# Kernel optimization log

Hardware: AMD Instinct MI355X
Metric: run time of the kernel (lower is better)

Reference implementation:

```python
import jax, jax.numpy as jnp
import numpy as np

N_NODES = 50000
N_EDGES = 800000
NFEAT, NHID, NCLASS, NCLUSTER = 512, 64, 16, 32


def gcn_conv(x, W, b, edge_index, edge_weight, n):
    """PyG GCNConv: add self-loops, symmetric normalization, linear + scatter-add."""
    row, col = edge_index[0], edge_index[1]
    loop = jnp.arange(n, dtype=row.dtype)
    row = jnp.concatenate([row, loop])
    col = jnp.concatenate([col, loop])
    w = jnp.concatenate([edge_weight, jnp.ones((n,), dtype=edge_weight.dtype)])
    # degree computed on target index (gcn_norm convention)
    deg = jax.ops.segment_sum(w, col, num_segments=n)
    dinv = jnp.where(deg > 0, jax.lax.rsqrt(deg), 0.0)
    norm = dinv[row] * w * dinv[col]          # [E+n]
    xw = x @ W                                # [n, out]
    msg = xw[row] * norm[:, None]             # gather + scale
    out = jax.ops.segment_sum(msg, col, num_segments=n)  # scatter-add
    return out + b


def setup_inputs() -> dict:
    key = jax.random.key(0)
    ks = jax.random.split(key, 12)
    def glorot(k, fan_in, fan_out):
        s = np.sqrt(6.0 / (fan_in + fan_out)).astype(np.float32)
        return jax.random.uniform(k, (fan_in, fan_out), jnp.float32, -s, s)
    x = jax.random.normal(ks[0], (N_NODES, NFEAT), jnp.float32)
    edge_index = jax.random.randint(ks[1], (2, N_EDGES), 0, N_NODES, dtype=jnp.int64)
    edge_weight = jax.random.uniform(ks[2], (N_EDGES,), jnp.float32)
    return {
        "x": x, "edge_index": edge_index, "edge_weight": edge_weight,
        "W1": glorot(ks[3], NFEAT, NHID), "b1": jnp.zeros((NHID,), jnp.float32),
        "W2": glorot(ks[4], NHID, NHID), "b2": jnp.zeros((NHID,), jnp.float32),
        "fcW1": glorot(ks[5], NHID, NCLASS), "fcb1": jnp.zeros((NCLASS,), jnp.float32),
        "fcW2": glorot(ks[6], NHID, NCLUSTER), "fcb2": jnp.zeros((NCLUSTER,), jnp.float32),
    }


def reference(x, edge_index, edge_weight, W1, b1, W2, b2, fcW1, fcb1, fcW2, fcb2):
    n = x.shape[0]
    h = jax.nn.relu(gcn_conv(x, W1, b1, edge_index, edge_weight, n))
    # dropout omitted (eval-mode / deterministic reference)
    h = gcn_conv(h, W2, b2, edge_index, edge_weight, n)
    pred = h @ fcW1 + fcb1
    pred_cluster = h @ fcW2 + fcb2
    return (pred, pred_cluster)
```

## Files before the change

### kernel.cpp

```cpp
#include <hip/hip_runtime.h>
#include <hip/hip_bf16.h>
#include <cstdint>
#include <cstddef>

#define N_FEAT 512
#define N_HID 64
#define N_CLASS 16
#define N_CLUSTER 32
#define NPART 8

typedef short short8 __attribute__((ext_vector_type(8)));
typedef float floatx4 __attribute__((ext_vector_type(4)));
typedef unsigned short u16;
typedef unsigned short u16x4 __attribute__((ext_vector_type(4)));

__device__ __forceinline__ short f2bf(float f) {
  __hip_bfloat16 h = __float2bfloat16(f);
  return *reinterpret_cast<short*>(&h);
}
__device__ __forceinline__ u16 f2bfu(float f) { return (u16)f2bf(f); }
__device__ __forceinline__ float bf2f(u16 u) {
  return __uint_as_float((unsigned)u << 16);
}

__global__ void k_zeroH(uint4* __restrict__ p, int n16) {
  int i = blockIdx.x * 256 + threadIdx.x;
  if (i < n16) p[i] = make_uint4(0u, 0u, 0u, 0u);
}

__global__ void k_degcnt2(const int* __restrict__ col, const float* __restrict__ w,
                          unsigned long long* __restrict__ hist, int H, int E) {
  int e = blockIdx.x * 256 + threadIdx.x;
  if (e >= E) return;
  int p = blockIdx.x & (NPART - 1);
  int c = col[e];
  unsigned long long fx = (unsigned long long)__float2uint_rn(w[e] * 16777216.0f);
  atomicAdd(&hist[(size_t)p * H + c], (1ull << 40) | fx);
}

__global__ void k_reduce(const unsigned long long* __restrict__ hist, int H,
                         int* __restrict__ cnt, float* __restrict__ dinv, int n) {
  int i = blockIdx.x * 256 + threadIdx.x;
  if (i >= n) return;
  unsigned long long tot = 0;
  #pragma unroll
  for (int p = 0; p < NPART; ++p) tot += hist[(size_t)p * H + i];
  int c = (int)(tot >> 40);
  float wsum = (float)(tot & ((1ull << 40) - 1)) * 5.9604644775390625e-08f;
  cnt[i] = c;
  dinv[i] = rsqrtf(1.0f + wsum);
}

__global__ __launch_bounds__(256) void k_scan1(const int* __restrict__ cnt,
                                               int* __restrict__ off,
                                               int* __restrict__ bsum, int n) {
  __shared__ int sh[256];
  int t = threadIdx.x;
  int i = blockIdx.x * 256 + t;
  int v = (i < n) ? cnt[i] : 0;
  sh[t] = v;
  __syncthreads();
  #pragma unroll
  for (int d = 1; d < 256; d <<= 1) {
    int x = 0;
    if (t >= d) x = sh[t - d];
    __syncthreads();
    if (t >= d) sh[t] += x;
    __syncthreads();
  }
  if (i < n) off[i] = sh[t] - v;
  if (t == 255) bsum[blockIdx.x] = sh[255];
}

__global__ __launch_bounds__(256) void k_scan2(const int* __restrict__ bsum,
                                               int* __restrict__ bsum2, int nb) {
  __shared__ int sh[256];
  int t = threadIdx.x;
  int v = (t < nb) ? bsum[t] : 0;
  sh[t] = v;
  __syncthreads();
  #pragma unroll
  for (int d = 1; d < 256; d <<= 1) {
    int x = 0;
    if (t >= d) x = sh[t - d];
    __syncthreads();
    if (t >= d) sh[t] += x;
    __syncthreads();
  }
  if (t < nb) bsum2[t] = sh[t] - v;
}

__global__ void k_scan3_initcur(int* __restrict__ off, const int* __restrict__ bsum2,
                                const unsigned long long* __restrict__ hist, int H,
                                int* __restrict__ cur, int n, int E) {
  int i = blockIdx.x * 256 + threadIdx.x;
  if (i < n) {
    int o = off[i] + bsum2[blockIdx.x];
    off[i] = o;
    int running = o;
    #pragma unroll
    for (int p = 0; p < NPART; ++p) {
      cur[(size_t)p * H + i] = running;
      running += (int)(hist[(size_t)p * H + i] >> 40);
    }
  }
  if (i == 0) off[n] = E;
}

__global__ void k_fill2(const int* __restrict__ rowi, const int* __restrict__ coli,
                        const float* __restrict__ w, const float* __restrict__ dinv,
                        int* __restrict__ cur, int H,
                        unsigned* __restrict__ pairs, int E) {
  int e = blockIdx.x * 256 + threadIdx.x;
  if (e >= E) return;
  int p = blockIdx.x & (NPART - 1);
  int r = rowi[e], c = coli[e];
  int pos = atomicAdd(&cur[(size_t)p * H + c], 1);
  unsigned pk = ((unsigned)r << 16) | (u16)f2bf(dinv[r] * w[e] * dinv[c]);
  pairs[pos] = pk;
}

__global__ void k_prepBF(const float* __restrict__ W, short* __restrict__ BF, int K) {
  int idx = blockIdx.x * 256 + threadIdx.x;
  int total = (K / 32) * 4 * 64;
  if (idx >= total) return;
  int lane = idx & 63;
  int sj = idx >> 6;
  int j = sj & 3, s = sj >> 2;
  int col = j * 16 + (lane & 15);
  int k0 = s * 32 + ((lane >> 4) << 3);
  short8 v;
  #pragma unroll
  for (int t = 0; t < 8; ++t) v[t] = f2bf(W[(size_t)(k0 + t) * 64 + col]);
  *(short8*)(BF + (size_t)idx * 8) = v;
}

template<int K, bool ABF>
__global__ __launch_bounds__(64, 4) void k_mfma(
    const void* __restrict__ Av, const short8* __restrict__ BF,
    u16* __restrict__ C, int M) {
  constexpr int NSTEP = K / 32;
  constexpr int PA = (NSTEP < 4) ? NSTEP : 4;
  constexpr int PB = (NSTEP < 2) ? NSTEP : 2;
  const int lane = threadIdx.x & 63;
  const int rbase = blockIdx.x * 16;
  int r = rbase + (lane & 15);
  if (r >= M) r = M - 1;
  const int klo = (lane >> 4) * 8;
  const float* arowf = (const float*)Av + (size_t)r * K + klo;
  const u16*   arowh = (const u16*)Av + (size_t)r * K + klo;
  const short8* bbase = BF + lane;

  float4 pa0[PA], pa1[PA];
  short8 pah[PA];
  short8 pb[PB][4];
  #pragma unroll
  for (int s = 0; s < PA; ++s) {
    if constexpr (ABF) {
      pah[s] = *(const short8*)(arowh + s * 32);
    } else {
      pa0[s] = *(const float4*)(arowf + s * 32);
      pa1[s] = *(const float4*)(arowf + s * 32 + 4);
    }
  }
  #pragma unroll
  for (int s = 0; s < PB; ++s) {
    #pragma unroll
    for (int j = 0; j < 4; ++j)
      pb[s][j] = bbase[(s * 4 + j) * 64];
  }
  __builtin_amdgcn_sched_barrier(0);

  floatx4 acc[4];
  #pragma unroll
  for (int j = 0; j < 4; ++j) acc[j] = (floatx4){0.f, 0.f, 0.f, 0.f};

  #pragma unroll
  for (int s = 0; s < NSTEP; ++s) {
    const int sa = s % PA;
    const int sb = s % PB;
    short8 af;
    if constexpr (ABF) {
      af = pah[sa];
    } else {
      float4 a0 = pa0[sa], a1 = pa1[sa];
      af[0] = f2bf(a0.x); af[1] = f2bf(a0.y); af[2] = f2bf(a0.z); af[3] = f2bf(a0.w);
      af[4] = f2bf(a1.x); af[5] = f2bf(a1.y); af[6] = f2bf(a1.z); af[7] = f2bf(a1.w);
    }
    acc[0] = __builtin_amdgcn_mfma_f32_16x16x32_bf16(af, pb[sb][0], acc[0], 0, 0, 0);
    acc[1] = __builtin_amdgcn_mfma_f32_16x16x32_bf16(af, pb[sb][1], acc[1], 0, 0, 0);
    acc[2] = __builtin_amdgcn_mfma_f32_16x16x32_bf16(af, pb[sb][2], acc[2], 0, 0, 0);
    acc[3] = __builtin_amdgcn_mfma_f32_16x16x32_bf16(af, pb[sb][3], acc[3], 0, 0, 0);
    if (s + PA < NSTEP) {
      if constexpr (ABF) {
        pah[sa] = *(const short8*)(arowh + (s + PA) * 32);
      } else {
        pa0[sa] = *(const float4*)(arowf + (s + PA) * 32);
        pa1[sa] = *(const float4*)(arowf + (s + PA) * 32 + 4);
      }
    }
    if (s + PB < NSTEP) {
      #pragma unroll
      for (int j = 0; j < 4; ++j)
        pb[sb][j] = bbase[((s + PB) * 4 + j) * 64];
    }
    __builtin_amdgcn_sched_barrier(0);
  }

  const int srow = rbase + (lane >> 4) * 4;
  const int scol = lane & 15;
  #pragma unroll
  for (int i = 0; i < 4; ++i) {
    int rr = srow + i;
    if (rr < M) {
      #pragma unroll
      for (int j = 0; j < 4; ++j)
        C[(size_t)rr * 64 + j * 16 + scol] = f2bfu(acc[j][i]);
    }
  }
}

template<bool RELU>
__global__ __launch_bounds__(256) void k_gather(
    const int* __restrict__ off, const unsigned* __restrict__ pairs,
    const float* __restrict__ dinv,
    const u16* __restrict__ xw, const float* __restrict__ bias,
    u16* __restrict__ h, int n) {
  int gid = blockIdx.x * 256 + threadIdx.x;
  int c = gid >> 6, lane = gid & 63;
  if (c >= n) return;
  float s = dinv[c]; s *= s;
  float acc = fmaf(bf2f(xw[(size_t)c * 64 + lane]), s, bias[lane]);
  int i = off[c], end = off[c + 1];
  for (; i + 7 < end; i += 8) {
    unsigned p[8];
    float v[8];
    #pragma unroll
    for (int t = 0; t < 8; ++t) p[t] = pairs[i + t];
    #pragma unroll
    for (int t = 0; t < 8; ++t)
      v[t] = bf2f(xw[(size_t)(p[t] >> 16) * 64 + lane]);
    #pragma unroll
    for (int t = 0; t < 8; ++t)
      acc = fmaf(v[t], __uint_as_float((p[t] & 0xffffu) << 16), acc);
  }
  for (; i + 1 < end; i += 2) {
    unsigned p0 = pairs[i], p1 = pairs[i + 1];
    float v0 = bf2f(xw[(size_t)(p0 >> 16) * 64 + lane]);
    float v1 = bf2f(xw[(size_t)(p1 >> 16) * 64 + lane]);
    acc = fmaf(v0, __uint_as_float((p0 & 0xffffu) << 16), acc);
    acc = fmaf(v1, __uint_as_float((p1 & 0xffffu) << 16), acc);
  }
  if (i < end) {
    unsigned p = pairs[i];
    acc = fmaf(bf2f(xw[(size_t)(p >> 16) * 64 + lane]),
               __uint_as_float((p & 0xffffu) << 16), acc);
  }
  if (RELU) acc = fmaxf(acc, 0.f);
  h[(size_t)c * 64 + lane] = f2bfu(acc);
}

__global__ __launch_bounds__(256) void k_fc(
    const u16* __restrict__ h,
    const float* __restrict__ fW1, const float* __restrict__ fb1,
    const float* __restrict__ fW2, const float* __restrict__ fb2,
    float* __restrict__ out, int M) {
  __shared__ float Hs[64][68];
  __shared__ float Ws[64][48];
  __shared__ float bs[48];
  const int t = threadIdx.x;
  const int row0 = blockIdx.x * 64;
  #pragma unroll
  for (int i = 0; i < 4; ++i) {
    int f = t + i * 256;
    int r = f >> 4, k4 = f & 15;
    int rr = row0 + r;
    float4 v = make_float4(0.f, 0.f, 0.f, 0.f);
    if (rr < M) {
      u16x4 u = *(const u16x4*)&h[(size_t)rr * 64 + k4 * 4];
      v = make_float4(bf2f(u[0]), bf2f(u[1]), bf2f(u[2]), bf2f(u[3]));
    }
    *(float4*)&Hs[r][k4 * 4] = v;
  }
  for (int f = t; f < 64 * 48; f += 256) {
    int k = f / 48, c = f - k * 48;
    Ws[k][c] = (c < 16) ? fW1[k * 16 + c] : fW2[k * 32 + (c - 16)];
  }
  if (t < 48) bs[t] = (t < 16) ? fb1[t] : fb2[t - 16];
  __syncthreads();
  const int tr = t >> 4, tc = t & 15;
  float acc[4][3] = {{0.f}};
  #pragma unroll 8
  for (int k = 0; k < 64; ++k) {
    float a[4], b[3];
    #pragma unroll
    for (int i = 0; i < 4; ++i) a[i] = Hs[tr * 4 + i][k];
    #pragma unroll
    for (int j = 0; j < 3; ++j) b[j] = Ws[k][tc * 3 + j];
    #pragma unroll
    for (int i = 0; i < 4; ++i)
      #pragma unroll
      for (int j = 0; j < 3; ++j) acc[i][j] = fmaf(a[i], b[j], acc[i][j]);
  }
  #pragma unroll
  for (int i = 0; i < 4; ++i) {
    int rr = row0 + tr * 4 + i;
    if (rr >= M) continue;
    #pragma unroll
    for (int j = 0; j < 3; ++j) {
      int c = tc * 3 + j;
      float v = acc[i][j] + bs[c];
      if (c < 16) out[(size_t)rr * 16 + c] = v;
      else out[(size_t)M * 16 + (size_t)rr * 32 + (c - 16)] = v;
    }
  }
}

extern "C" void kernel_launch(void* const* d_in, const int* in_sizes, int n_in,
                              void* d_out, int out_size, void* d_ws, size_t ws_size,
                              hipStream_t stream) {
  const float* x    = (const float*)d_in[0];
  const int*   ei   = (const int*)d_in[1];
  const float* ew   = (const float*)d_in[2];
  const float* W1   = (const float*)d_in[3];
  const float* b1   = (const float*)d_in[4];
  const float* W2   = (const float*)d_in[5];
  const float* b2   = (const float*)d_in[6];
  const float* fW1  = (const float*)d_in[7];
  const float* fb1  = (const float*)d_in[8];
  const float* fW2  = (const float*)d_in[9];
  const float* fb2  = (const float*)d_in[10];
  float* out = (float*)d_out;

  const int N = in_sizes[0] / N_FEAT;
  const int E = in_sizes[2];
  const int H = (N + 63) & ~63;
  const int* row = ei;
  const int* col = ei + E;

  char* ws = (char*)d_ws;
  float*              dinv = (float*)(ws + 0x000000);
  int*                cnt  = (int*)  (ws + 0x040000);
  int*                off  = (int*)  (ws + 0x080000);
  int*                bsum = (int*)  (ws + 0x0C0000);
  int*                bsum2= (int*)  (ws + 0x0C1000);
  short*              BF1  = (short*)(ws + 0x0C8000);
  short*              BF2  = (short*)(ws + 0x0DA000);
  unsigned long long* hist = (unsigned long long*)(ws + 0x100000);
  int*                cur  = (int*)  (ws + 0x500000);
  unsigned*           pairs= (unsigned*)(ws + 0x6C0000);
  u16*                bufA = (u16*)  (ws + 0xD40000);
  u16*                bufB = (u16*)  (ws + 0x1980000);

  const int nbN  = (N + 255) / 256;
  const int nbE  = (E + 255) / 256;
  const int nbT  = (N + 15) / 16;
  const int nbG  = (N + 63) / 64;
  const int nbW  = (N * 64 + 255) / 256;
  const int nH16 = NPART * H / 2;
  const int nbZ  = (nH16 + 255) / 256;

  k_prepBF<<<32, 256, 0, stream>>>(W1, BF1, N_FEAT);
  k_prepBF<<<2,  256, 0, stream>>>(W2, BF2, N_HID);

  k_zeroH  <<<nbZ, 256, 0, stream>>>((uint4*)hist, nH16);
  k_degcnt2<<<nbE, 256, 0, stream>>>(col, ew, hist, H, E);
  k_reduce <<<nbN, 256, 0, stream>>>(hist, H, cnt, dinv, N);
  k_scan1  <<<nbN, 256, 0, stream>>>(cnt, off, bsum, N);
  k_scan2  <<<1,   256, 0, stream>>>(bsum, bsum2, nbN);
  k_scan3_initcur<<<nbN, 256, 0, stream>>>(off, bsum2, hist, H, cur, N, E);
  k_fill2  <<<nbE, 256, 0, stream>>>(row, col, ew, dinv, cur, H, pairs, E);

  k_mfma<N_FEAT, false><<<nbT, 64, 0, stream>>>(x, (const short8*)BF1, bufA, N);
  k_gather<true><<<nbW, 256, 0, stream>>>(off, pairs, dinv, bufA, b1, bufB, N);

  k_mfma<N_HID, true><<<nbT, 64, 0, stream>>>(bufB, (const short8*)BF2, bufA, N);
  k_gather<false><<<nbW, 256, 0, stream>>>(off, pairs, dinv, bufA, b2, bufB, N);

  k_fc<<<nbG, 256, 0, stream>>>(bufB, fW1, fb1, fW2, fb2, out, N);
}
```

Baseline: 196.6 us.

## Stage x tiles through swizzled LDS with double buffering in first GEMM

Replaces the single-wave 16-row MFMA kernel for the 512-wide input projection with a 256-thread, 64-row block. Each block streams 64-column fp32 chunks of x into XOR-swizzled double-buffered shared memory with coalesced loads, then each wave converts to bf16 and issues MFMAs while the next chunk loads. The K=64 second GEMM is split into its own simplified kernel. The aim is better global-load coalescing and more memory parallelism on the 100MB x read, at the cost of barriers and LDS traffic.

```diff
diff --git a/kernel.cpp b/kernel.cpp
--- a/kernel.cpp
+++ b/kernel.cpp
@@ -135,76 +135,123 @@
   *(short8*)(BF + (size_t)idx * 8) = v;
 }
 
-template<int K, bool ABF>
-__global__ __launch_bounds__(64, 4) void k_mfma(
-    const void* __restrict__ Av, const short8* __restrict__ BF,
+__global__ __launch_bounds__(256, 3) void k_mfma512(
+    const float* __restrict__ A, const short8* __restrict__ BF,
     u16* __restrict__ C, int M) {
-  constexpr int NSTEP = K / 32;
-  constexpr int PA = (NSTEP < 4) ? NSTEP : 4;
-  constexpr int PB = (NSTEP < 2) ? NSTEP : 2;
+  __shared__ float As[2][4096];
+  const int tid = threadIdx.x;
+  const int lane = tid & 63;
+  const int wid = tid >> 6;
+  const int row0 = blockIdx.x * 64;
+
+  const int srow = tid >> 4;
+  const int scol4 = (tid & 15) ^ (srow & 7);
+  const float* gsrc[4];
+  #pragma unroll
+  for (int i = 0; i < 4; ++i) {
+    int grow = row0 + i * 16 + srow;
+    if (grow >= M) grow = M - 1;
+    gsrc[i] = A + (size_t)grow * 512 + scol4 * 4;
+  }
+  const int ldsoff = tid * 4;
+
+  const int row_r = wid * 16 + (lane & 15);
+  const int xr = row_r & 7;
+  const int kqb = (lane >> 4) * 2;
+
+  float4 st[4];
+  short8 pb[2][8];
+  floatx4 acc[4];
+  #pragma unroll
+  for (int j = 0; j < 4; ++j) acc[j] = (floatx4){0.f, 0.f, 0.f, 0.f};
+
+  #pragma unroll
+  for (int i = 0; i < 4; ++i) st[i] = *(const float4*)(gsrc[i]);
+  #pragma unroll
+  for (int t = 0; t < 8; ++t) pb[0][t] = BF[t * 64 + lane];
+  #pragma unroll
+  for (int i = 0; i < 4; ++i)
+    *(float4*)&As[0][i * 1024 + ldsoff] = st[i];
+  __syncthreads();
+
+  #pragma unroll
+  for (int c = 0; c < 8; ++c) {
+    const int b = c & 1;
+    if (c + 1 < 8) {
+      #pragma unroll
+      for (int i = 0; i < 4; ++i)
+        st[i] = *(const float4*)(gsrc[i] + (c + 1) * 64);
+      #pragma unroll
+      for (int t = 0; t < 8; ++t)
+        pb[b ^ 1][t] = BF[((c + 1) * 8 + t) * 64 + lane];
+      __builtin_amdgcn_sched_barrier(0);
+    }
+    const float* rb = &As[b][row_r * 64];
+    #pragma unroll
+    for (int kq = 0; kq < 2; ++kq) {
+      const int k4a = kq * 8 + kqb;
+      float4 f0 = *(const float4*)&rb[((k4a)     ^ xr) * 4];
+      float4 f1 = *(const float4*)&rb[((k4a + 1) ^ xr) * 4];
+      short8 af;
+      af[0] = f2bf(f0.x); af[1] = f2bf(f0.y); af[2] = f2bf(f0.z); af[3] = f2bf(f0.w);
+      af[4] = f2bf(f1.x); af[5] = f2bf(f1.y); af[6] = f2bf(f1.z); af[7] = f2bf(f1.w);
+      acc[0] = __builtin_amdgcn_mfma_f32_16x16x32_bf16(af, pb[b][kq * 4 + 0], acc[0], 0, 0, 0);
+      acc[1] = __builtin_amdgcn_mfma_f32_16x16x32_bf16(af, pb[b][kq * 4 + 1], acc[1], 0, 0, 0);
+      acc[2] = __builtin_amdgcn_mfma_f32_16x16x32_bf16(af, pb[b][kq * 4 + 2], acc[2], 0, 0, 0);
+      acc[3] = __builtin_amdgcn_mfma_f32_16x16x32_bf16(af, pb[b][kq * 4 + 3], acc[3], 0, 0, 0);
+    }
+    if (c + 1 < 8) {
+      #pragma unroll
+      for (int i = 0; i < 4; ++i)
+        *(float4*)&As[b ^ 1][i * 1024 + ldsoff] = st[i];
+      __syncthreads();
+    }
+  }
+
+  const int srowo = row0 + wid * 16 + (lane >> 4) * 4;
+  const int scol = lane & 15;
+  #pragma unroll
+  for (int i = 0; i < 4; ++i) {
+    int rr = srowo + i;
+    if (rr < M) {
+      #pragma unroll
+      for (int j = 0; j < 4; ++j)
+        C[(size_t)rr * 64 + j * 16 + scol] = f2bfu(acc[j][i]);
+    }
+  }
+}
+
+__global__ __launch_bounds__(64, 4) void k_mfma64(
+    const u16* __restrict__ Av, const short8* __restrict__ BF,
+    u16* __restrict__ C, int M) {
   const int lane = threadIdx.x & 63;
   const int rbase = blockIdx.x * 16;
   int r = rbase + (lane & 15);
   if (r >= M) r = M - 1;
   const int klo = (lane >> 4) * 8;
-  const float* arowf = (const float*)Av + (size_t)r * K + klo;
-  const u16*   arowh = (const u16*)Av + (size_t)r * K + klo;
+  const u16* arow = Av + (size_t)r * 64 + klo;
   const short8* bbase = BF + lane;
 
-  float4 pa0[PA], pa1[PA];
-  short8 pah[PA];
-  short8 pb[PB][4];
-  #pragma unroll
-  for (int s = 0; s < PA; ++s) {
-    if constexpr (ABF) {
-      pah[s] = *(const short8*)(arowh + s * 32);
-    } else {
-      pa0[s] = *(const float4*)(arowf + s * 32);
-      pa1[s] = *(const float4*)(arowf + s * 32 + 4);
-    }
-  }
-  #pragma unroll
-  for (int s = 0; s < PB; ++s) {
+  short8 pah[2];
+  short8 pb[2][4];
+  pah[0] = *(const short8*)(arow);
+  pah[1] = *(const short8*)(arow + 32);
+  #pragma unroll
+  for (int s = 0; s < 2; ++s)
     #pragma unroll
     for (int j = 0; j < 4; ++j)
       pb[s][j] = bbase[(s * 4 + j) * 64];
-  }
-  __builtin_amdgcn_sched_barrier(0);
 
   floatx4 acc[4];
   #pragma unroll
   for (int j = 0; j < 4; ++j) acc[j] = (floatx4){0.f, 0.f, 0.f, 0.f};
 
   #pragma unroll
-  for (int s = 0; s < NSTEP; ++s) {
-    const int sa = s % PA;
-    const int sb = s % PB;
-    short8 af;
-    if constexpr (ABF) {
-      af = pah[sa];
-    } else {
-      float4 a0 = pa0[sa], a1 = pa1[sa];
-      af[0] = f2bf(a0.x); af[1] = f2bf(a0.y); af[2] = f2bf(a0.z); af[3] = f2bf(a0.w);
-      af[4] = f2bf(a1.x); af[5] = f2bf(a1.y); af[6] = f2bf(a1.z); af[7] = f2bf(a1.w);
-    }
-    acc[0] = __builtin_amdgcn_mfma_f32_16x16x32_bf16(af, pb[sb][0], acc[0], 0, 0, 0);
-    acc[1] = __builtin_amdgcn_mfma_f32_16x16x32_bf16(af, pb[sb][1], acc[1], 0, 0, 0);
-    acc[2] = __builtin_amdgcn_mfma_f32_16x16x32_bf16(af, pb[sb][2], acc[2], 0, 0, 0);
-    acc[3] = __builtin_amdgcn_mfma_f32_16x16x32_bf16(af, pb[sb][3], acc[3], 0, 0, 0);
-    if (s + PA < NSTEP) {
-      if constexpr (ABF) {
-        pah[sa] = *(const short8*)(arowh + (s + PA) * 32);
-      } else {
-        pa0[sa] = *(const float4*)(arowf + (s + PA) * 32);
-        pa1[sa] = *(const float4*)(arowf + (s + PA) * 32 + 4);
-      }
-    }
-    if (s + PB < NSTEP) {
-      #pragma unroll
-      for (int j = 0; j < 4; ++j)
-        pb[sb][j] = bbase[((s + PB) * 4 + j) * 64];
-    }
-    __builtin_amdgcn_sched_barrier(0);
+  for (int s = 0; s < 2; ++s) {
+    acc[0] = __builtin_amdgcn_mfma_f32_16x16x32_bf16(pah[s], pb[s][0], acc[0], 0, 0, 0);
+    acc[1] = __builtin_amdgcn_mfma_f32_16x16x32_bf16(pah[s], pb[s][1], acc[1], 0, 0, 0);
+    acc[2] = __builtin_amdgcn_mfma_f32_16x16x32_bf16(pah[s], pb[s][2], acc[2], 0, 0, 0);
+    acc[3] = __builtin_amdgcn_mfma_f32_16x16x32_bf16(pah[s], pb[s][3], acc[3], 0, 0, 0);
   }
 
   const int srow = rbase + (lane >> 4) * 4;
@@ -354,6 +401,7 @@
 
   const int nbN  = (N + 255) / 256;
   const int nbE  = (E + 255) / 256;
+  const int nbS  = (N + 63) / 64;
   const int nbT  = (N + 15) / 16;
   const int nbG  = (N + 63) / 64;
   const int nbW  = (N * 64 + 255) / 256;
@@ -371,10 +419,10 @@
   k_scan3_initcur<<<nbN, 256, 0, stream>>>(off, bsum2, hist, H, cur, N, E);
   k_fill2  <<<nbE, 256, 0, stream>>>(row, col, ew, dinv, cur, H, pairs, E);
 
-  k_mfma<N_FEAT, false><<<nbT, 64, 0, stream>>>(x, (const short8*)BF1, bufA, N);
+  k_mfma512<<<nbS, 256, 0, stream>>>(x, (const short8*)BF1, bufA, N);
   k_gather<true><<<nbW, 256, 0, stream>>>(off, pairs, dinv, bufA, b1, bufB, N);
 
-  k_mfma<N_HID, true><<<nbT, 64, 0, stream>>>(bufB, (const short8*)BF2, bufA, N);
+  k_mfma64<<<nbT, 64, 0, stream>>>(bufB, (const short8*)BF2, bufA, N);
   k_gather<false><<<nbW, 256, 0, stream>>>(off, pairs, dinv, bufA, b2, bufB, N);
 
   k_fc<<<nbG, 256, 0, stream>>>(bufB, fW1, fb1, fW2, fb2, out, N);
```

After: 196.3 us. No clear change (-0.2%).

## Split first GEMM along K into four partial kernels and fuse reduce with scan

Applied to the files above, without the earlier changes.

The first X·W1 GEMM (K=512) is split into four K-chunks of 128, each launched as its own set of wave blocks writing bf16 partial results. A new combine kernel then sums the partials into the final buffer. The aim is to expose four times more parallelism and memory-level concurrency for the 100 MB input read. The degree reduce and first scan stage are merged into one kernel, dropping the cnt buffer and one launch. The cost is an extra launch, extra partial-buffer traffic (about 25 MB written and read), and an extra bf16 rounding step on each partial.

```diff
diff --git a/kernel.cpp b/kernel.cpp
--- a/kernel.cpp
+++ b/kernel.cpp
@@ -8,11 +8,13 @@
 #define N_CLASS 16
 #define N_CLUSTER 32
 #define NPART 8
+#define KSPLIT 4
 
 typedef short short8 __attribute__((ext_vector_type(8)));
 typedef float floatx4 __attribute__((ext_vector_type(4)));
 typedef unsigned short u16;
 typedef unsigned short u16x4 __attribute__((ext_vector_type(4)));
+typedef unsigned short u16x8 __attribute__((ext_vector_type(8)));
 
 __device__ __forceinline__ short f2bf(float f) {
   __hip_bfloat16 h = __float2bfloat16(f);
@@ -38,26 +40,22 @@
   atomicAdd(&hist[(size_t)p * H + c], (1ull << 40) | fx);
 }
 
-__global__ void k_reduce(const unsigned long long* __restrict__ hist, int H,
-                         int* __restrict__ cnt, float* __restrict__ dinv, int n) {
-  int i = blockIdx.x * 256 + threadIdx.x;
-  if (i >= n) return;
-  unsigned long long tot = 0;
-  #pragma unroll
-  for (int p = 0; p < NPART; ++p) tot += hist[(size_t)p * H + i];
-  int c = (int)(tot >> 40);
-  float wsum = (float)(tot & ((1ull << 40) - 1)) * 5.9604644775390625e-08f;
-  cnt[i] = c;
-  dinv[i] = rsqrtf(1.0f + wsum);
-}
-
-__global__ __launch_bounds__(256) void k_scan1(const int* __restrict__ cnt,
-                                               int* __restrict__ off,
-                                               int* __restrict__ bsum, int n) {
+__global__ __launch_bounds__(256) void k_redscan(
+    const unsigned long long* __restrict__ hist, int H,
+    float* __restrict__ dinv, int* __restrict__ off,
+    int* __restrict__ bsum, int n) {
   __shared__ int sh[256];
   int t = threadIdx.x;
   int i = blockIdx.x * 256 + t;
-  int v = (i < n) ? cnt[i] : 0;
+  int v = 0;
+  if (i < n) {
+    unsigned long long tot = 0;
+    #pragma unroll
+    for (int p = 0; p < NPART; ++p) tot += hist[(size_t)p * H + i];
+    v = (int)(tot >> 40);
+    float wsum = (float)(tot & ((1ull << 40) - 1)) * 5.9604644775390625e-08f;
+    dinv[i] = rsqrtf(1.0f + wsum);
+  }
   sh[t] = v;
   __syncthreads();
   #pragma unroll
@@ -116,8 +114,7 @@
   int p = blockIdx.x & (NPART - 1);
   int r = rowi[e], c = coli[e];
   int pos = atomicAdd(&cur[(size_t)p * H + c], 1);
-  unsigned pk = ((unsigned)r << 16) | (u16)f2bf(dinv[r] * w[e] * dinv[c]);
-  pairs[pos] = pk;
+  pairs[pos] = ((unsigned)r << 16) | (u16)f2bf(dinv[r] * w[e] * dinv[c]);
 }
 
 __global__ void k_prepBF(const float* __restrict__ W, short* __restrict__ BF, int K) {
@@ -135,76 +132,115 @@
   *(short8*)(BF + (size_t)idx * 8) = v;
 }
 
-template<int K, bool ABF>
-__global__ __launch_bounds__(64, 4) void k_mfma(
-    const void* __restrict__ Av, const short8* __restrict__ BF,
+__global__ __launch_bounds__(64, 5) void k_mfma128(
+    const float* __restrict__ A, const short8* __restrict__ BF,
+    u16* __restrict__ Cp, int M, int nbT) {
+  const int q = blockIdx.x / nbT;
+  const int tb = blockIdx.x - q * nbT;
+  const int lane = threadIdx.x & 63;
+  const int rbase = tb * 16;
+  int r = rbase + (lane & 15);
+  if (r >= M) r = M - 1;
+  const float* arow = A + (size_t)r * 512 + q * 128 + ((lane >> 4) << 3);
+  const short8* bbase = BF + q * 1024 + lane;
+
+  float4 a[8];
+  #pragma unroll
+  for (int s = 0; s < 4; ++s) {
+    a[2 * s]     = *(const float4*)(arow + s * 32);
+    a[2 * s + 1] = *(const float4*)(arow + s * 32 + 4);
+  }
+  short8 pb[2][4];
+  #pragma unroll
+  for (int s = 0; s < 2; ++s)
+    #pragma unroll
+    for (int j = 0; j < 4; ++j)
+      pb[s][j] = bbase[(s * 4 + j) * 64];
+  __builtin_amdgcn_sched_barrier(0);
+
+  floatx4 acc[4];
+  #pragma unroll
+  for (int j = 0; j < 4; ++j) acc[j] = (floatx4){0.f, 0.f, 0.f, 0.f};
+
+  #pragma unroll
+  for (int s = 0; s < 4; ++s) {
+    const int sb = s & 1;
+    float4 a0 = a[2 * s], a1 = a[2 * s + 1];
+    short8 af;
+    af[0] = f2bf(a0.x); af[1] = f2bf(a0.y); af[2] = f2bf(a0.z); af[3] = f2bf(a0.w);
+    af[4] = f2bf(a1.x); af[5] = f2bf(a1.y); af[6] = f2bf(a1.z); af[7] = f2bf(a1.w);
+    acc[0] = __builtin_amdgcn_mfma_f32_16x16x32_bf16(af, pb[sb][0], acc[0], 0, 0, 0);
+    acc[1] = __builtin_amdgcn_mfma_f32_16x16x32_bf16(af, pb[sb][1], acc[1], 0, 0, 0);
+    acc[2] = __builtin_amdgcn_mfma_f32_16x16x32_bf16(af, pb[sb][2], acc[2], 0, 0, 0);
+    acc[3] = __builtin_amdgcn_mfma_f32_16x16x32_bf16(af, pb[sb][3], acc[3], 0, 0, 0);
+    if (s + 2 < 4) {
+      #pragma unroll
+      for (int j = 0; j < 4; ++j)
+        pb[sb][j] = bbase[((s + 2) * 4 + j) * 64];
+    }
+    __builtin_amdgcn_sched_barrier(0);
+  }
+
+  u16* Cq = Cp + (size_t)q * M * 64;
+  const int srow = rbase + (lane >> 4) * 4;
+  const int scol = lane & 15;
+  #pragma unroll
+  for (int i = 0; i < 4; ++i) {
+    int rr = srow + i;
+    if (rr < M) {
+      #pragma unroll
+      for (int j = 0; j < 4; ++j)
+        Cq[(size_t)rr * 64 + j * 16 + scol] = f2bfu(acc[j][i]);
+    }
+  }
+}
+
+__global__ void k_comb(const u16* __restrict__ Cp, u16* __restrict__ Cf,
+                       int n8, int part) {
+  int i = blockIdx.x * 256 + threadIdx.x;
+  if (i >= n8) return;
+  u16x8 p0 = *(const u16x8*)(Cp + (size_t)i * 8);
+  u16x8 p1 = *(const u16x8*)(Cp + (size_t)part + i * 8);
+  u16x8 p2 = *(const u16x8*)(Cp + (size_t)2 * part + i * 8);
+  u16x8 p3 = *(const u16x8*)(Cp + (size_t)3 * part + i * 8);
+  u16x8 o;
+  #pragma unroll
+  for (int j = 0; j < 8; ++j)
+    o[j] = f2bfu((bf2f(p0[j]) + bf2f(p1[j])) + (bf2f(p2[j]) + bf2f(p3[j])));
+  *(u16x8*)(Cf + (size_t)i * 8) = o;
+}
+
+__global__ __launch_bounds__(64, 4) void k_mfma64(
+    const u16* __restrict__ Av, const short8* __restrict__ BF,
     u16* __restrict__ C, int M) {
-  constexpr int NSTEP = K / 32;
-  constexpr int PA = (NSTEP < 4) ? NSTEP : 4;
-  constexpr int PB = (NSTEP < 2) ? NSTEP : 2;
   const int lane = threadIdx.x & 63;
   const int rbase = blockIdx.x * 16;
   int r = rbase + (lane & 15);
   if (r >= M) r = M - 1;
   const int klo = (lane >> 4) * 8;
-  const float* arowf = (const float*)Av + (size_t)r * K + klo;
-  const u16*   arowh = (const u16*)Av + (size_t)r * K + klo;
+  const u16* arow = Av + (size_t)r * 64 + klo;
   const short8* bbase = BF + lane;
 
-  float4 pa0[PA], pa1[PA];
-  short8 pah[PA];
-  short8 pb[PB][4];
-  #pragma unroll
-  for (int s = 0; s < PA; ++s) {
-    if constexpr (ABF) {
-      pah[s] = *(const short8*)(arowh + s * 32);
-    } else {
-      pa0[s] = *(const float4*)(arowf + s * 32);
-      pa1[s] = *(const float4*)(arowf + s * 32 + 4);
-    }
-  }
-  #pragma unroll
-  for (int s = 0; s < PB; ++s) {
+  short8 pah[2];
+  short8 pb[2][4];
+  pah[0] = *(const short8*)(arow);
+  pah[1] = *(const short8*)(arow + 32);
+  #pragma unroll
+  for (int s = 0; s < 2; ++s)
     #pragma unroll
     for (int j = 0; j < 4; ++j)
       pb[s][j] = bbase[(s * 4 + j) * 64];
-  }
-  __builtin_amdgcn_sched_barrier(0);
 
   floatx4 acc[4];
   #pragma unroll
   for (int j = 0; j < 4; ++j) acc[j] = (floatx4){0.f, 0.f, 0.f, 0.f};
 
   #pragma unroll
-  for (int s = 0; s < NSTEP; ++s) {
-    const int sa = s % PA;
-    const int sb = s % PB;
-    short8 af;
-    if constexpr (ABF) {
-      af = pah[sa];
-    } else {
-      float4 a0 = pa0[sa], a1 = pa1[sa];
-      af[0] = f2bf(a0.x); af[1] = f2bf(a0.y); af[2] = f2bf(a0.z); af[3] = f2bf(a0.w);
-      af[4] = f2bf(a1.x); af[5] = f2bf(a1.y); af[6] = f2bf(a1.z); af[7] = f2bf(a1.w);
-    }
-    acc[0] = __builtin_amdgcn_mfma_f32_16x16x32_bf16(af, pb[sb][0], acc[0], 0, 0, 0);
-    acc[1] = __builtin_amdgcn_mfma_f32_16x16x32_bf16(af, pb[sb][1], acc[1], 0, 0, 0);
-    acc[2] = __builtin_amdgcn_mfma_f32_16x16x32_bf16(af, pb[sb][2], acc[2], 0, 0, 0);
-    acc[3] = __builtin_amdgcn_mfma_f32_16x16x32_bf16(af, pb[sb][3], acc[3], 0, 0, 0);
-    if (s + PA < NSTEP) {
-      if constexpr (ABF) {
-        pah[sa] = *(const short8*)(arowh + (s + PA) * 32);
-      } else {
-        pa0[sa] = *(const float4*)(arowf + (s + PA) * 32);
-        pa1[sa] = *(const float4*)(arowf + (s + PA) * 32 + 4);
-      }
-    }
-    if (s + PB < NSTEP) {
-      #pragma unroll
-      for (int j = 0; j < 4; ++j)
-        pb[sb][j] = bbase[((s + PB) * 4 + j) * 64];
-    }
-    __builtin_amdgcn_sched_barrier(0);
+  for (int s = 0; s < 2; ++s) {
+    acc[0] = __builtin_amdgcn_mfma_f32_16x16x32_bf16(pah[s], pb[s][0], acc[0], 0, 0, 0);
+    acc[1] = __builtin_amdgcn_mfma_f32_16x16x32_bf16(pah[s], pb[s][1], acc[1], 0, 0, 0);
+    acc[2] = __builtin_amdgcn_mfma_f32_16x16x32_bf16(pah[s], pb[s][2], acc[2], 0, 0, 0);
+    acc[3] = __builtin_amdgcn_mfma_f32_16x16x32_bf16(pah[s], pb[s][3], acc[3], 0, 0, 0);
   }
 
   const int srow = rbase + (lane >> 4) * 4;
@@ -340,7 +376,6 @@
 
   char* ws = (char*)d_ws;
   float*              dinv = (float*)(ws + 0x000000);
-  int*                cnt  = (int*)  (ws + 0x040000);
   int*                off  = (int*)  (ws + 0x080000);
   int*                bsum = (int*)  (ws + 0x0C0000);
   int*                bsum2= (int*)  (ws + 0x0C1000);
@@ -349,8 +384,9 @@
   unsigned long long* hist = (unsigned long long*)(ws + 0x100000);
   int*                cur  = (int*)  (ws + 0x500000);
   unsigned*           pairs= (unsigned*)(ws + 0x6C0000);
-  u16*                bufA = (u16*)  (ws + 0xD40000);
-  u16*                bufB = (u16*)  (ws + 0x1980000);
+  u16*                Cp   = (u16*)  (ws + 0xA00000);
+  u16*                bufA = (u16*)  (ws + 0x2400000);
+  u16*                bufB = (u16*)  (ws + 0x2B00000);
 
   const int nbN  = (N + 255) / 256;
   const int nbE  = (E + 255) / 256;
@@ -359,22 +395,24 @@
   const int nbW  = (N * 64 + 255) / 256;
   const int nH16 = NPART * H / 2;
   const int nbZ  = (nH16 + 255) / 256;
+  const int n8   = N * 64 / 8;
+  const int nbC  = (n8 + 255) / 256;
 
   k_prepBF<<<32, 256, 0, stream>>>(W1, BF1, N_FEAT);
   k_prepBF<<<2,  256, 0, stream>>>(W2, BF2, N_HID);
 
   k_zeroH  <<<nbZ, 256, 0, stream>>>((uint4*)hist, nH16);
   k_degcnt2<<<nbE, 256, 0, stream>>>(col, ew, hist, H, E);
-  k_reduce <<<nbN, 256, 0, stream>>>(hist, H, cnt, dinv, N);
-  k_scan1  <<<nbN, 256, 0, stream>>>(cnt, off, bsum, N);
+  k_redscan<<<nbN, 256, 0, stream>>>(hist, H, dinv, off, bsum, N);
   k_scan2  <<<1,   256, 0, stream>>>(bsum, bsum2, nbN);
   k_scan3_initcur<<<nbN, 256, 0, stream>>>(off, bsum2, hist, H, cur, N, E);
   k_fill2  <<<nbE, 256, 0, stream>>>(row, col, ew, dinv, cur, H, pairs, E);
 
-  k_mfma<N_FEAT, false><<<nbT, 64, 0, stream>>>(x, (const short8*)BF1, bufA, N);
+  k_mfma128<<<KSPLIT * nbT, 64, 0, stream>>>(x, (const short8*)BF1, Cp, N, nbT);
+  k_comb   <<<nbC, 256, 0, stream>>>(Cp, bufA, n8, N * 64);
   k_gather<true><<<nbW, 256, 0, stream>>>(off, pairs, dinv, bufA, b1, bufB, N);
 
-  k_mfma<N_HID, true><<<nbT, 64, 0, stream>>>(bufB, (const short8*)BF2, bufA, N);
+  k_mfma64<<<nbT, 64, 0, stream>>>(bufB, (const short8*)BF2, bufA, N);
   k_gather<false><<<nbW, 256, 0, stream>>>(off, pairs, dinv, bufA, b2, bufB, N);
 
   k_fc<<<nbG, 256, 0, stream>>>(bufB, fW1, fb1, fW2, fb2, out, N);
```

After: 203.7 us. 3.6% more time.
